# Optimization experiments

Hardware: AMD Instinct MI355X
Metric: run time of the kernel (lower is better)

Reference implementation:

```python
import jax, jax.numpy as jnp
import numpy as np
import math
from functools import lru_cache

LMAX = 2
MUL = 64
BATCH = 1024
# all parity-allowed paths for lmax=2, in the module's enumeration order
PATHS = [(0,0,0),(0,1,1),(0,2,2),(1,0,1),(1,1,0),(1,1,2),(1,2,1),(2,0,2),(2,1,1),(2,2,0),(2,2,2)]

# ---- CG tensor construction (numpy, float64), faithful port of the torch source ----

def _counts(L):
    return [(a, b, L - a - b) for a in range(L, -1, -1) for b in range(L - a, -1, -1)]

def _dfact(n):
    out = 1
    for k in range(n, 0, -2):
        out *= k
    return out

def _gmom(n):
    return 0.0 if n % 2 == 1 else float(_dfact(n - 1))

@lru_cache(maxsize=None)
def _gram(L):
    c = _counts(L)
    D = len(c)
    G = np.zeros((D, D))
    for i, (a, b, cc) in enumerate(c):
        for j, (a2, b2, c2) in enumerate(c):
            G[i, j] = _gmom(a + a2) * _gmom(b + b2) * _gmom(cc + c2)
    return G

@lru_cache(maxsize=None)
def _laplacian(L):
    cL = _counts(L)
    cS = _counts(L - 2)
    idxS = {t: i for i, t in enumerate(cS)}
    M = np.zeros((len(cS), len(cL)))
    for j, (a, b, c) in enumerate(cL):
        if a >= 2: M[idxS[(a - 2, b, c)], j] += a * (a - 1)
        if b >= 2: M[idxS[(a, b - 2, c)], j] += b * (b - 1)
        if c >= 2: M[idxS[(a, b, c - 2)], j] += c * (c - 1)
    return M

@lru_cache(maxsize=None)
def _harm_basis(L):
    # harmonic basis in monomial coords: null space of Laplacian, whitened by Gaussian Gram
    if L == 0:
        return np.ones((1, 1))
    if L == 1:
        return np.eye(3)
    Delta = _laplacian(L)
    _, s, vh = np.linalg.svd(Delta, full_matrices=True)
    rank = int((s > 1e-12).sum())
    B = vh[rank:].T
    G = _gram(L)
    M = B.T @ G @ B
    ev, evec = np.linalg.eigh(M)
    ev = np.clip(ev, 1e-14, None)
    W = evec @ np.diag(ev ** -0.5) @ evec.T
    return B @ W

@lru_cache(maxsize=None)
def _r2k_lift(l, k):
    # multiply Sym^l polynomial by (x^2+y^2+z^2)^k -> Sym^{l+2k}
    cl = _counts(l)
    cL = _counts(l + 2 * k)
    idxL = {t: i for i, t in enumerate(cL)}
    M = np.zeros((len(cL), len(cl)))
    for i in range(k + 1):
        for j in range(k - i + 1):
            h = k - i - j
            coef = math.factorial(k) / (math.factorial(i) * math.factorial(j) * math.factorial(h))
            for col, (a, b, c) in enumerate(cl):
                M[idxL[(a + 2 * i, b + 2 * j, c + 2 * h)], col] += coef
    return M

@lru_cache(maxsize=None)
def _poly_mult(l1, l2, L):
    c1, c2, cL = _counts(l1), _counts(l2), _counts(L)
    idxL = {t: i for i, t in enumerate(cL)}
    M = np.zeros((len(cL), len(c1) * len(c2)))
    for i, a in enumerate(c1):
        for j, b in enumerate(c2):
            M[idxL[(a[0] + b[0], a[1] + b[1], a[2] + b[2])], i * len(c2) + j] = 1.0
    return M

@lru_cache(maxsize=None)
def _projector(L, l):
    # P_{L->l}: monomial coeffs of Sym^L -> harmonic coords of Harm^l
    k = (L - l) // 2
    GL = _gram(L)
    Bl = _harm_basis(l)
    V = _r2k_lift(l, k) @ Bl
    G = V.T @ GL @ V
    return np.linalg.solve(G, V.T @ GL)

@lru_cache(maxsize=None)
def _cg(l1, l2, l3):
    L = l1 + l2
    P = _projector(L, l3)
    B1, B2 = _harm_basis(l1), _harm_basis(l2)
    Mp = _poly_mult(l1, l2, L)
    m1, m2 = 2 * l1 + 1, 2 * l2 + 1
    outer = np.einsum('im,jn->ijmn', B1, B2).reshape(B1.shape[0] * B2.shape[0], m1 * m2)
    C = (P @ (Mp @ outer)).T.reshape(m1, m2, 2 * l3 + 1)
    n = np.linalg.norm(C)
    if n > 1e-30:  # 'component' normalization
        C = C * (math.sqrt(2 * l3 + 1) / n)
    return C


def setup_inputs() -> dict:
    key = jax.random.key(0)
    ks = jax.random.split(key, 7)
    inp = {}
    for l in range(LMAX + 1):
        inp[f'x1_l{l}'] = jax.random.normal(ks[l], (BATCH, MUL, 2 * l + 1), dtype=jnp.float32)
        inp[f'x2_l{l}'] = jax.random.normal(ks[l + 3], (BATCH, MUL, 2 * l + 1), dtype=jnp.float32)
    inp['W'] = jax.random.normal(ks[6], (len(PATHS), MUL, MUL, MUL), dtype=jnp.float32) * 0.02
    for p, (l1, l2, l3) in enumerate(PATHS):
        inp[f'C_{p}'] = jnp.asarray(_cg(l1, l2, l3), dtype=jnp.float32)
    return inp


def reference(x1_l0, x1_l1, x1_l2, x2_l0, x2_l1, x2_l2, W,
              C_0, C_1, C_2, C_3, C_4, C_5, C_6, C_7, C_8, C_9, C_10):
    x1 = {0: x1_l0, 1: x1_l1, 2: x1_l2}
    x2 = {0: x2_l0, 1: x2_l1, 2: x2_l2}
    Cs = [C_0, C_1, C_2, C_3, C_4, C_5, C_6, C_7, C_8, C_9, C_10]
    B = x1_l0.shape[0]
    mul_out = W.shape[1]
    out = {l: jnp.zeros((B, mul_out, 2 * l + 1), dtype=x1_l0.dtype) for l in range(LMAX + 1)}
    for p, (l1, l2, l3) in enumerate(PATHS):
        # out[z,w,k] += sum_{u,v,m,n} x1[z,u,m] x2[z,v,n] W[p,w,u,v] C[p][m,n,k]
        out[l3] = out[l3] + jnp.einsum('zum,zvn,wuv,mnk->zwk',
                                       x1[l1], x2[l2], W[p], Cs[p], optimize='optimal')
    # concatenate the output irrep dict l -> (B, mul_out, 2l+1) along the m axis
    return jnp.concatenate([out[l] for l in range(LMAX + 1)], axis=-1)
```

## Files before the change

### kernel.cpp

```cpp
#include <hip/hip_runtime.h>
#include <hip/hip_bf16.h>


#define NTHREADS 256
#define SMEM_BYTES 51456

typedef __attribute__((ext_vector_type(4))) float f32x4;
typedef __attribute__((ext_vector_type(8))) short s16x8;

__device__ __forceinline__ unsigned short f2bf(float x) {
    union { float f; unsigned u; } v; v.f = x;
    unsigned r = v.u + 0x7fffu + ((v.u >> 16) & 1u);
    return (unsigned short)(r >> 16);
}
__device__ __forceinline__ unsigned pk2bf(float a, float b) {
    union { __hip_bfloat162 h; unsigned u; } v;
    v.h = __float22bfloat162_rn(make_float2(a, b));
    return v.u;
}


__global__ __launch_bounds__(NTHREADS) void prep_w(const float* __restrict__ W,
                                                   unsigned short* __restrict__ Wb)
{
    int id = blockIdx.x * NTHREADS + threadIdx.x;
    int v4 = (id & 15) << 2;
    int w  = (id >> 4) & 63;
    int u  = (id >> 10) & 63;
    int p  = id >> 16;
    float4 f = *(const float4*)(W + (((size_t)p * 64 + w) * 64 + u) * 64 + v4);
    ushort4 h;
    h.x = f2bf(f.x); h.y = f2bf(f.y); h.z = f2bf(f.z); h.w = f2bf(f.w);
    *(ushort4*)(Wb + (((size_t)p * 64 + u) * 64 + w) * 64 + v4) = h;
}


struct KArgs {
    const float*          x1[3];
    const float*          x2[3];
    const unsigned short* Wb;
    const float*          C[11];
    float*                part[11];
};

template <int M1, int N1, int K1, int ZT, int S1, int UC>
__device__ __forceinline__ void run_path(const float* __restrict__ x1g,
                                         const float* __restrict__ x2g,
                                         const unsigned short* __restrict__ Wbp,
                                         const float* __restrict__ Cg,
                                         float* __restrict__ partp,
                                         int local, char* __restrict__ smem)
{
    constexpr int KN   = K1 * N1;
    constexpr int NC   = ZT * K1 / 16;
    constexpr bool EVEN = (NC % 2 == 0);
    constexpr int ROWT = EVEN ? 2 : 1;
    constexpr int COLT = EVEN ? NC / 2 : NC;
    constexpr int PASSES = ZT / 8;
    constexpr int SST  = UC * S1 + 4;
    constexpr int TROWS = ZT * K1;
    static_assert(512 + ZT * SST * 4 + 2 * TROWS * 136 * 2 <= SMEM_BYTES, "LDS");

    float*          sC  = (float*)smem;
    float*          sc1 = (float*)(smem + 512);
    unsigned short* sT0 = (unsigned short*)(smem + 512 + ZT * SST * 4);

    const int t = threadIdx.x, lane = t & 63, wave = t >> 6;
    const int ln = lane & 15, q = lane >> 4;
    const int zz = lane >> 5, vp = lane & 31;
    const int ztile = local >> 2, usub = local & 3;
    const int z0 = ztile * ZT, u0 = usub * 16;

    for (int i = t; i < M1 * N1 * K1; i += NTHREADS) sC[i] = Cg[i];
    __syncthreads();

    auto build_slab = [&](int us0) {
        for (int i = t; i < ZT * UC * KN; i += NTHREADS) {
            int z   = i / (UC * KN);
            int r   = i - z * (UC * KN);
            int uu2 = r / KN;
            int j   = r - uu2 * KN;
            int k   = j / N1, n = j - k * N1;
            const float* x1r = x1g + ((size_t)(z0 + z) * 64 + u0 + us0 + uu2) * M1;
            float s = 0.f;
#pragma unroll
            for (int m = 0; m < M1; ++m) s += x1r[m] * sC[(m * N1 + n) * K1 + k];
            sc1[z * SST + uu2 * S1 + j] = s;
        }
    };

    float xr[PASSES][2][N1];
#pragma unroll
    for (int p = 0; p < PASSES; ++p) {
        const int z = z0 + p * 8 + wave * 2 + zz;
        const float* xp = x2g + ((size_t)z * 64 + 2 * vp) * N1;
#pragma unroll
        for (int j = 0; j < 2 * N1; ++j) xr[p][j / N1][j % N1] = xp[j];
    }

    auto tform = [&](int uf, unsigned short* sTn) {
        const int uus = uf % UC;
        const int coff = (uf & 1) * 64 + 2 * vp;
#pragma unroll
        for (int p = 0; p < PASSES; ++p) {
            const int z = p * 8 + wave * 2 + zz;
            const float4* cp = (const float4*)&sc1[z * SST + uus * S1];
            float c1v[S1];
#pragma unroll
            for (int jj = 0; jj < S1 / 4; ++jj) {
                float4 f = cp[jj];
                c1v[jj * 4 + 0] = f.x; c1v[jj * 4 + 1] = f.y;
                c1v[jj * 4 + 2] = f.z; c1v[jj * 4 + 3] = f.w;
            }
#pragma unroll
            for (int k = 0; k < K1; ++k) {
                float s0 = 0.f, s1 = 0.f;
#pragma unroll
                for (int n = 0; n < N1; ++n) {
                    const float cv = c1v[k * N1 + n];
                    s0 += xr[p][0][n] * cv;
                    s1 += xr[p][1][n] * cv;
                }
                *(unsigned*)&sTn[(z * K1 + k) * 136 + coff] = pk2bf(s0, s1);
            }
        }
    };

    f32x4 acc[ROWT][COLT];
#pragma unroll
    for (int rt = 0; rt < ROWT; ++rt)
#pragma unroll
        for (int ci = 0; ci < COLT; ++ci) acc[rt][ci] = (f32x4){0.f, 0.f, 0.f, 0.f};

    build_slab(0);
    __syncthreads();
    tform(0, sT0);
    tform(1, sT0);
    __syncthreads();

#pragma unroll 1
    for (int it = 0; it < 8; ++it) {
        if (((2 * it + 2) % UC) == 0 && it < 7) {
            build_slab(2 * it + 2);
            __syncthreads();
        }
        const int cur = it & 1;
        unsigned short* sTc = sT0 + cur * (TROWS * 136);
        unsigned short* sTn = sT0 + (cur ^ 1) * (TROWS * 136);

        s16x8 areg[ROWT][4];
#pragma unroll
        for (int us = 0; us < 2; ++us) {
            const unsigned short* wsrc = Wbp + (size_t)(u0 + 2 * it + us) * 4096;
#pragma unroll
            for (int rt = 0; rt < ROWT; ++rt) {
                const int wt = EVEN ? ((wave >> 1) * 2 + rt) : wave;
#pragma unroll
                for (int s2 = 0; s2 < 2; ++s2)
                    areg[rt][us * 2 + s2] =
                        *(const s16x8*)(wsrc + (wt * 16 + ln) * 64 + s2 * 32 + q * 8);
            }
        }

        if (it < 7) { tform(2 * it + 2, sTn); tform(2 * it + 3, sTn); }

#pragma unroll
        for (int ci = 0; ci < COLT; ++ci) {
            const int c = EVEN ? ((wave & 1) * COLT + ci) : ci;
            const unsigned short* brow = &sTc[(c * 16 + ln) * 136];
#pragma unroll
            for (int c4 = 0; c4 < 4; ++c4) {
                s16x8 bf = *(const s16x8*)(brow + c4 * 32 + q * 8);
#pragma unroll
                for (int rt = 0; rt < ROWT; ++rt)
                    acc[rt][ci] = __builtin_amdgcn_mfma_f32_16x16x32_bf16(
                        areg[rt][c4], bf, acc[rt][ci], 0, 0, 0);
            }
        }
        __syncthreads();
    }

#pragma unroll
    for (int rt = 0; rt < ROWT; ++rt) {
        const int wt = EVEN ? ((wave >> 1) * 2 + rt) : wave;
#pragma unroll
        for (int ci = 0; ci < COLT; ++ci) {
            const int c = EVEN ? ((wave & 1) * COLT + ci) : ci;
            const int col = c * 16 + ln;
            const int z = col / K1, k = col - z * K1;
            float* op = partp + ((size_t)(usub * 1024 + z0 + z) * 64) * K1 + k;
#pragma unroll
            for (int r = 0; r < 4; ++r)
                op[(wt * 16 + q * 4 + r) * K1] = acc[rt][ci][r];
        }
    }
}

__global__ __launch_bounds__(NTHREADS, 3) void tp_main(KArgs a)
{
    __shared__ __align__(16) char smem[SMEM_BYTES];

    const int bid = blockIdx.x;
    const int starts[12] = {0, 256, 512, 768, 1024, 1280, 1536, 1792, 2048, 2176, 2304, 2432};
    int idx = 0;
#pragma unroll
    for (int i = 1; i < 12; ++i) idx += (bid >= starts[i]) ? 1 : 0;
    const int local = bid - starts[idx];

    switch (idx) {
        case 0:  run_path<1,5,5,16,28, 4>(a.x1[0], a.x2[2], a.Wb + (size_t) 2*262144, a.C[2],  a.part[2],  local, smem); break;
        case 1:  run_path<5,5,5,16,28, 4>(a.x1[2], a.x2[2], a.Wb + (size_t)10*262144, a.C[10], a.part[10], local, smem); break;
        case 2:  run_path<3,3,5,16,16, 4>(a.x1[1], a.x2[1], a.Wb + (size_t) 5*262144, a.C[5],  a.part[5],  local, smem); break;
        case 3:  run_path<5,1,5,16, 8, 8>(a.x1[2], a.x2[0], a.Wb + (size_t) 7*262144, a.C[7],  a.part[7],  local, smem); break;
        case 4:  run_path<3,5,3,16,16, 8>(a.x1[1], a.x2[2], a.Wb + (size_t) 6*262144, a.C[6],  a.part[6],  local, smem); break;
        case 5:  run_path<1,3,3,16,12, 8>(a.x1[0], a.x2[1], a.Wb + (size_t) 1*262144, a.C[1],  a.part[1],  local, smem); break;
        case 6:  run_path<5,3,3,16,12, 8>(a.x1[2], a.x2[1], a.Wb + (size_t) 8*262144, a.C[8],  a.part[8],  local, smem); break;
        case 7:  run_path<3,1,3,16, 4,16>(a.x1[1], a.x2[0], a.Wb + (size_t) 3*262144, a.C[3],  a.part[3],  local, smem); break;
        case 8:  run_path<5,5,1,32, 8,16>(a.x1[2], a.x2[2], a.Wb + (size_t) 9*262144, a.C[9],  a.part[9],  local, smem); break;
        case 9:  run_path<3,3,1,32, 4,16>(a.x1[1], a.x2[1], a.Wb + (size_t) 4*262144, a.C[4],  a.part[4],  local, smem); break;
        case 10: run_path<1,1,1,32, 4,16>(a.x1[0], a.x2[0], a.Wb + (size_t) 0*262144, a.C[0],  a.part[0],  local, smem); break;
        default: break;
    }
}


struct RArgs {
    const float* part[11];
    float*       out;
};

__global__ __launch_bounds__(NTHREADS) void reduce_out(RArgs r)
{
    const int g   = blockIdx.x >> 8;
    const int tid = (blockIdx.x & 255) * NTHREADS + threadIdx.x;
    float* op = r.out + (size_t)tid * 9;

    if (g == 0) {
        const int P[3] = {0, 4, 9};
        float o = 0.f;
#pragma unroll
        for (int pi = 0; pi < 3; ++pi) {
            const float* pp = r.part[P[pi]];
#pragma unroll
            for (int us = 0; us < 4; ++us)
                o += pp[(size_t)(us * 65536) + tid];
        }
        op[0] = o;
    } else if (g == 1) {
        const int P[4] = {1, 3, 6, 8};
        float o[3] = {0.f, 0.f, 0.f};
#pragma unroll
        for (int pi = 0; pi < 4; ++pi) {
            const float* pp = r.part[P[pi]];
#pragma unroll
            for (int us = 0; us < 4; ++us) {
                const float* row = pp + ((size_t)(us * 65536) + tid) * 3;
#pragma unroll
                for (int k = 0; k < 3; ++k) o[k] += row[k];
            }
        }
#pragma unroll
        for (int k = 0; k < 3; ++k) op[1 + k] = o[k];
    } else {
        const int P[4] = {2, 5, 7, 10};
        float o[5] = {0.f, 0.f, 0.f, 0.f, 0.f};
#pragma unroll
        for (int pi = 0; pi < 4; ++pi) {
            const float* pp = r.part[P[pi]];
#pragma unroll
            for (int us = 0; us < 4; ++us) {
                const float* row = pp + ((size_t)(us * 65536) + tid) * 5;
#pragma unroll
                for (int k = 0; k < 5; ++k) o[k] += row[k];
            }
        }
#pragma unroll
        for (int k = 0; k < 5; ++k) op[4 + k] = o[k];
    }
}


extern "C" void kernel_launch(void* const* d_in, const int* in_sizes, int n_in,
                              void* d_out, int out_size, void* d_ws, size_t ws_size,
                              hipStream_t stream)
{
    static const int cumK1[11] = {0, 1, 4, 9, 12, 13, 18, 21, 26, 29, 30};

    unsigned short* Wb = (unsigned short*)d_ws;
    float* partbase = (float*)((char*)d_ws + (6u << 20));

    KArgs a;
    a.x1[0] = (const float*)d_in[0];
    a.x2[0] = (const float*)d_in[1];
    a.x1[1] = (const float*)d_in[2];
    a.x2[1] = (const float*)d_in[3];
    a.x1[2] = (const float*)d_in[4];
    a.x2[2] = (const float*)d_in[5];
    a.Wb = Wb;
    RArgs rr;
    for (int p = 0; p < 11; ++p) {
        a.C[p]    = (const float*)d_in[7 + p];
        a.part[p] = partbase + (size_t)cumK1[p] * 262144;
        rr.part[p] = a.part[p];
    }
    rr.out = (float*)d_out;

    prep_w<<<dim3(720896 / NTHREADS), NTHREADS, 0, stream>>>((const float*)d_in[6], Wb);
    tp_main<<<dim3(2432), NTHREADS, 0, stream>>>(a);
    reduce_out<<<dim3(768), NTHREADS, 0, stream>>>(rr);
}
```

Measured before the change: 184.6 us.

## Form MFMA B operand in registers and split the v dimension across blocks

Restructures the per-path kernel so each lane builds its bf16 B fragment for the MFMA directly in registers from x2 and the bf16 CG-contracted x1 slab. This removes the shared-memory double-buffered transformed tile and its extra syncs. Blocks now cover 32 u by 32 v with larger z tiles, which lowers the grid from 2432 to 960 blocks and shrinks LDS. The slab is stored in bf16, adding rounding, and the output partial layout changes to slice = usub*2+vh, which must match what the reduce kernel expects.

```diff
diff --git a/kernel.cpp b/kernel.cpp
--- a/kernel.cpp
+++ b/kernel.cpp
@@ -3,7 +3,7 @@
 
 
 #define NTHREADS 256
-#define SMEM_BYTES 51456
+#define SMEM_BYTES 34304
 
 typedef __attribute__((ext_vector_type(4))) float f32x4;
 typedef __attribute__((ext_vector_type(8))) short s16x8;
@@ -12,6 +12,10 @@
     union { float f; unsigned u; } v; v.f = x;
     unsigned r = v.u + 0x7fffu + ((v.u >> 16) & 1u);
     return (unsigned short)(r >> 16);
+}
+__device__ __forceinline__ float bf2f(unsigned short h) {
+    union { unsigned u; float f; } v; v.u = ((unsigned)h) << 16;
+    return v.f;
 }
 __device__ __forceinline__ unsigned pk2bf(float a, float b) {
     union { __hip_bfloat162 h; unsigned u; } v;
@@ -43,7 +47,7 @@
     float*                part[11];
 };
 
-template <int M1, int N1, int K1, int ZT, int S1, int UC>
+template <int M1, int N1, int K1, int ROWT, int KNP>
 __device__ __forceinline__ void run_path(const float* __restrict__ x1g,
                                          const float* __restrict__ x2g,
                                          const unsigned short* __restrict__ Wbp,
@@ -52,147 +56,132 @@
                                          int local, char* __restrict__ smem)
 {
     constexpr int KN   = K1 * N1;
-    constexpr int NC   = ZT * K1 / 16;
-    constexpr bool EVEN = (NC % 2 == 0);
-    constexpr int ROWT = EVEN ? 2 : 1;
-    constexpr int COLT = EVEN ? NC / 2 : NC;
-    constexpr int PASSES = ZT / 8;
-    constexpr int SST  = UC * S1 + 4;
-    constexpr int TROWS = ZT * K1;
-    static_assert(512 + ZT * SST * 4 + 2 * TROWS * 136 * 2 <= SMEM_BYTES, "LDS");
+    constexpr int NB   = KNP / 8;
+    constexpr int ZG   = (ROWT == 2) ? 2 : 4;
+    constexpr int ZT   = ZG * 16;
+    constexpr int ZSTR = 16 * KNP + 8;
+    static_assert(KN <= KNP && KNP % 8 == 0, "");
+    static_assert(512 + ZT * ZSTR * 2 <= SMEM_BYTES, "LDS");
 
     float*          sC  = (float*)smem;
-    float*          sc1 = (float*)(smem + 512);
-    unsigned short* sT0 = (unsigned short*)(smem + 512 + ZT * SST * 4);
+    unsigned short* sc1 = (unsigned short*)(smem + 512);
 
     const int t = threadIdx.x, lane = t & 63, wave = t >> 6;
     const int ln = lane & 15, q = lane >> 4;
-    const int zz = lane >> 5, vp = lane & 31;
-    const int ztile = local >> 2, usub = local & 3;
-    const int z0 = ztile * ZT, u0 = usub * 16;
+    const int ztile = local >> 2;
+    const int usub = (local >> 1) & 1, vh = local & 1;
+    const int z0 = ztile * ZT, u0 = usub * 32;
+    const int wh = wave / ZG, zh = wave % ZG;
+    const int zloc = zh * 16 + ln;
+    const int zg = z0 + zloc;
+    const int v0 = vh * 32 + q * 8;
 
     for (int i = t; i < M1 * N1 * K1; i += NTHREADS) sC[i] = Cg[i];
+
+    float2 x2p[4][N1];
+#pragma unroll
+    for (int jj = 0; jj < 4; ++jj)
+#pragma unroll
+        for (int n = 0; n < N1; ++n)
+            x2p[jj][n] = make_float2(
+                x2g[((size_t)zg * 64 + v0 + 2 * jj) * N1 + n],
+                x2g[((size_t)zg * 64 + v0 + 2 * jj + 1) * N1 + n]);
+
+    f32x4 acc[ROWT][K1];
+#pragma unroll
+    for (int rt = 0; rt < ROWT; ++rt)
+#pragma unroll
+        for (int k = 0; k < K1; ++k) acc[rt][k] = (f32x4){0.f, 0.f, 0.f, 0.f};
+
     __syncthreads();
 
-    auto build_slab = [&](int us0) {
-        for (int i = t; i < ZT * UC * KN; i += NTHREADS) {
-            int z   = i / (UC * KN);
-            int r   = i - z * (UC * KN);
+#pragma unroll 1
+    for (int h = 0; h < 2; ++h) {
+        if (h) __syncthreads();
+        for (int i = t; i < ZT * 16 * KN; i += NTHREADS) {
+            int z   = i / (16 * KN);
+            int r   = i - z * (16 * KN);
             int uu2 = r / KN;
             int j   = r - uu2 * KN;
             int k   = j / N1, n = j - k * N1;
-            const float* x1r = x1g + ((size_t)(z0 + z) * 64 + u0 + us0 + uu2) * M1;
+            const float* x1r = x1g + ((size_t)(z0 + z) * 64 + u0 + h * 16 + uu2) * M1;
             float s = 0.f;
 #pragma unroll
             for (int m = 0; m < M1; ++m) s += x1r[m] * sC[(m * N1 + n) * K1 + k];
-            sc1[z * SST + uu2 * S1 + j] = s;
-        }
-    };
-
-    float xr[PASSES][2][N1];
-#pragma unroll
-    for (int p = 0; p < PASSES; ++p) {
-        const int z = z0 + p * 8 + wave * 2 + zz;
-        const float* xp = x2g + ((size_t)z * 64 + 2 * vp) * N1;
-#pragma unroll
-        for (int j = 0; j < 2 * N1; ++j) xr[p][j / N1][j % N1] = xp[j];
-    }
-
-    auto tform = [&](int uf, unsigned short* sTn) {
-        const int uus = uf % UC;
-        const int coff = (uf & 1) * 64 + 2 * vp;
-#pragma unroll
-        for (int p = 0; p < PASSES; ++p) {
-            const int z = p * 8 + wave * 2 + zz;
-            const float4* cp = (const float4*)&sc1[z * SST + uus * S1];
-            float c1v[S1];
-#pragma unroll
-            for (int jj = 0; jj < S1 / 4; ++jj) {
-                float4 f = cp[jj];
-                c1v[jj * 4 + 0] = f.x; c1v[jj * 4 + 1] = f.y;
-                c1v[jj * 4 + 2] = f.z; c1v[jj * 4 + 3] = f.w;
-            }
+            sc1[z * ZSTR + uu2 * KNP + j] = f2bf(s);
+        }
+        __syncthreads();
+
+        const unsigned short* cb = sc1 + zloc * ZSTR;
+
+        s16x8 cr[NB];
+#pragma unroll
+        for (int b = 0; b < NB; ++b) cr[b] = *(const s16x8*)(cb + b * 8);
+        s16x8 afc[ROWT];
+        {
+            const unsigned short* wsrc = Wbp + (size_t)(u0 + h * 16) * 4096;
+#pragma unroll
+            for (int rt = 0; rt < ROWT; ++rt)
+                afc[rt] = *(const s16x8*)(wsrc + ((wh * ROWT + rt) * 16 + ln) * 64 + v0);
+        }
+
+#pragma unroll 1
+        for (int uu = 0; uu < 16; ++uu) {
+            float c1v[KN];
+#pragma unroll
+            for (int j = 0; j < KN; ++j)
+                c1v[j] = bf2f((unsigned short)cr[j >> 3][j & 7]);
+
+            s16x8 afn[ROWT];
+            if (uu < 15) {
+#pragma unroll
+                for (int b = 0; b < NB; ++b)
+                    cr[b] = *(const s16x8*)(cb + (uu + 1) * KNP + b * 8);
+                const unsigned short* wsrc = Wbp + (size_t)(u0 + h * 16 + uu + 1) * 4096;
+#pragma unroll
+                for (int rt = 0; rt < ROWT; ++rt)
+                    afn[rt] = *(const s16x8*)(wsrc + ((wh * ROWT + rt) * 16 + ln) * 64 + v0);
+            }
+
 #pragma unroll
             for (int k = 0; k < K1; ++k) {
-                float s0 = 0.f, s1 = 0.f;
+                float2 s[4];
+#pragma unroll
+                for (int jj = 0; jj < 4; ++jj) s[jj] = make_float2(0.f, 0.f);
 #pragma unroll
                 for (int n = 0; n < N1; ++n) {
-                    const float cv = c1v[k * N1 + n];
-                    s0 += xr[p][0][n] * cv;
-                    s1 += xr[p][1][n] * cv;
+                    const float c = c1v[k * N1 + n];
+#pragma unroll
+                    for (int jj = 0; jj < 4; ++jj) {
+                        s[jj].x = fmaf(x2p[jj][n].x, c, s[jj].x);
+                        s[jj].y = fmaf(x2p[jj][n].y, c, s[jj].y);
+                    }
                 }
-                *(unsigned*)&sTn[(z * K1 + k) * 136 + coff] = pk2bf(s0, s1);
-            }
-        }
-    };
-
-    f32x4 acc[ROWT][COLT];
-#pragma unroll
-    for (int rt = 0; rt < ROWT; ++rt)
-#pragma unroll
-        for (int ci = 0; ci < COLT; ++ci) acc[rt][ci] = (f32x4){0.f, 0.f, 0.f, 0.f};
-
-    build_slab(0);
-    __syncthreads();
-    tform(0, sT0);
-    tform(1, sT0);
-    __syncthreads();
-
-#pragma unroll 1
-    for (int it = 0; it < 8; ++it) {
-        if (((2 * it + 2) % UC) == 0 && it < 7) {
-            build_slab(2 * it + 2);
-            __syncthreads();
-        }
-        const int cur = it & 1;
-        unsigned short* sTc = sT0 + cur * (TROWS * 136);
-        unsigned short* sTn = sT0 + (cur ^ 1) * (TROWS * 136);
-
-        s16x8 areg[ROWT][4];
-#pragma unroll
-        for (int us = 0; us < 2; ++us) {
-            const unsigned short* wsrc = Wbp + (size_t)(u0 + 2 * it + us) * 4096;
-#pragma unroll
-            for (int rt = 0; rt < ROWT; ++rt) {
-                const int wt = EVEN ? ((wave >> 1) * 2 + rt) : wave;
-#pragma unroll
-                for (int s2 = 0; s2 < 2; ++s2)
-                    areg[rt][us * 2 + s2] =
-                        *(const s16x8*)(wsrc + (wt * 16 + ln) * 64 + s2 * 32 + q * 8);
-            }
-        }
-
-        if (it < 7) { tform(2 * it + 2, sTn); tform(2 * it + 3, sTn); }
-
-#pragma unroll
-        for (int ci = 0; ci < COLT; ++ci) {
-            const int c = EVEN ? ((wave & 1) * COLT + ci) : ci;
-            const unsigned short* brow = &sTc[(c * 16 + ln) * 136];
-#pragma unroll
-            for (int c4 = 0; c4 < 4; ++c4) {
-                s16x8 bf = *(const s16x8*)(brow + c4 * 32 + q * 8);
+                union { uint4 u4; s16x8 v; } bf;
+                bf.u4 = make_uint4(pk2bf(s[0].x, s[0].y), pk2bf(s[1].x, s[1].y),
+                                   pk2bf(s[2].x, s[2].y), pk2bf(s[3].x, s[3].y));
 #pragma unroll
                 for (int rt = 0; rt < ROWT; ++rt)
-                    acc[rt][ci] = __builtin_amdgcn_mfma_f32_16x16x32_bf16(
-                        areg[rt][c4], bf, acc[rt][ci], 0, 0, 0);
-            }
-        }
-        __syncthreads();
-    }
-
+                    acc[rt][k] = __builtin_amdgcn_mfma_f32_16x16x32_bf16(
+                        afc[rt], bf.v, acc[rt][k], 0, 0, 0);
+            }
+            if (uu < 15) {
+#pragma unroll
+                for (int rt = 0; rt < ROWT; ++rt) afc[rt] = afn[rt];
+            }
+        }
+    }
+
+    const int slice = usub * 2 + vh;
+    float* opb = partp + ((size_t)(slice * 1024 + zg) * 64) * K1;
 #pragma unroll
     for (int rt = 0; rt < ROWT; ++rt) {
-        const int wt = EVEN ? ((wave >> 1) * 2 + rt) : wave;
-#pragma unroll
-        for (int ci = 0; ci < COLT; ++ci) {
-            const int c = EVEN ? ((wave & 1) * COLT + ci) : ci;
-            const int col = c * 16 + ln;
-            const int z = col / K1, k = col - z * K1;
-            float* op = partp + ((size_t)(usub * 1024 + z0 + z) * 64) * K1 + k;
+        const int wb = (wh * ROWT + rt) * 16 + q * 4;
+#pragma unroll
+        for (int k = 0; k < K1; ++k)
 #pragma unroll
             for (int r = 0; r < 4; ++r)
-                op[(wt * 16 + q * 4 + r) * K1] = acc[rt][ci][r];
-        }
+                opb[(wb + r) * K1 + k] = acc[rt][k][r];
     }
 }
 
@@ -201,24 +190,24 @@
     __shared__ __align__(16) char smem[SMEM_BYTES];
 
     const int bid = blockIdx.x;
-    const int starts[12] = {0, 256, 512, 768, 1024, 1280, 1536, 1792, 2048, 2176, 2304, 2432};
+    const int starts[12] = {0, 128, 256, 384, 512, 576, 640, 704, 768, 832, 896, 960};
     int idx = 0;
 #pragma unroll
     for (int i = 1; i < 12; ++i) idx += (bid >= starts[i]) ? 1 : 0;
     const int local = bid - starts[idx];
 
     switch (idx) {
-        case 0:  run_path<1,5,5,16,28, 4>(a.x1[0], a.x2[2], a.Wb + (size_t) 2*262144, a.C[2],  a.part[2],  local, smem); break;
-        case 1:  run_path<5,5,5,16,28, 4>(a.x1[2], a.x2[2], a.Wb + (size_t)10*262144, a.C[10], a.part[10], local, smem); break;
-        case 2:  run_path<3,3,5,16,16, 4>(a.x1[1], a.x2[1], a.Wb + (size_t) 5*262144, a.C[5],  a.part[5],  local, smem); break;
-        case 3:  run_path<5,1,5,16, 8, 8>(a.x1[2], a.x2[0], a.Wb + (size_t) 7*262144, a.C[7],  a.part[7],  local, smem); break;
-        case 4:  run_path<3,5,3,16,16, 8>(a.x1[1], a.x2[2], a.Wb + (size_t) 6*262144, a.C[6],  a.part[6],  local, smem); break;
-        case 5:  run_path<1,3,3,16,12, 8>(a.x1[0], a.x2[1], a.Wb + (size_t) 1*262144, a.C[1],  a.part[1],  local, smem); break;
-        case 6:  run_path<5,3,3,16,12, 8>(a.x1[2], a.x2[1], a.Wb + (size_t) 8*262144, a.C[8],  a.part[8],  local, smem); break;
-        case 7:  run_path<3,1,3,16, 4,16>(a.x1[1], a.x2[0], a.Wb + (size_t) 3*262144, a.C[3],  a.part[3],  local, smem); break;
-        case 8:  run_path<5,5,1,32, 8,16>(a.x1[2], a.x2[2], a.Wb + (size_t) 9*262144, a.C[9],  a.part[9],  local, smem); break;
-        case 9:  run_path<3,3,1,32, 4,16>(a.x1[1], a.x2[1], a.Wb + (size_t) 4*262144, a.C[4],  a.part[4],  local, smem); break;
-        case 10: run_path<1,1,1,32, 4,16>(a.x1[0], a.x2[0], a.Wb + (size_t) 0*262144, a.C[0],  a.part[0],  local, smem); break;
+        case 0:  run_path<1,5,5,2,32>(a.x1[0], a.x2[2], a.Wb + (size_t) 2*262144, a.C[2],  a.part[2],  local, smem); break;
+        case 1:  run_path<5,5,5,2,32>(a.x1[2], a.x2[2], a.Wb + (size_t)10*262144, a.C[10], a.part[10], local, smem); break;
+        case 2:  run_path<3,3,5,2,16>(a.x1[1], a.x2[1], a.Wb + (size_t) 5*262144, a.C[5],  a.part[5],  local, smem); break;
+        case 3:  run_path<5,1,5,2, 8>(a.x1[2], a.x2[0], a.Wb + (size_t) 7*262144, a.C[7],  a.part[7],  local, smem); break;
+        case 4:  run_path<3,5,3,4,16>(a.x1[1], a.x2[2], a.Wb + (size_t) 6*262144, a.C[6],  a.part[6],  local, smem); break;
+        case 5:  run_path<1,3,3,4,16>(a.x1[0], a.x2[1], a.Wb + (size_t) 1*262144, a.C[1],  a.part[1],  local, smem); break;
+        case 6:  run_path<5,3,3,4,16>(a.x1[2], a.x2[1], a.Wb + (size_t) 8*262144, a.C[8],  a.part[8],  local, smem); break;
+        case 7:  run_path<3,1,3,4, 8>(a.x1[1], a.x2[0], a.Wb + (size_t) 3*262144, a.C[3],  a.part[3],  local, smem); break;
+        case 8:  run_path<5,5,1,4, 8>(a.x1[2], a.x2[2], a.Wb + (size_t) 9*262144, a.C[9],  a.part[9],  local, smem); break;
+        case 9:  run_path<3,3,1,4, 8>(a.x1[1], a.x2[1], a.Wb + (size_t) 4*262144, a.C[4],  a.part[4],  local, smem); break;
+        case 10: run_path<1,1,1,4, 8>(a.x1[0], a.x2[0], a.Wb + (size_t) 0*262144, a.C[0],  a.part[0],  local, smem); break;
         default: break;
     }
 }
@@ -306,6 +295,6 @@
     rr.out = (float*)d_out;
 
     prep_w<<<dim3(720896 / NTHREADS), NTHREADS, 0, stream>>>((const float*)d_in[6], Wb);
-    tp_main<<<dim3(2432), NTHREADS, 0, stream>>>(a);
+    tp_main<<<dim3(960), NTHREADS, 0, stream>>>(a);
     reduce_out<<<dim3(768), NTHREADS, 0, stream>>>(rr);
 }
```

New measurement: 185.5 us. About the same (+0.5%).
